# Kernel tuning notes

Hardware: AMD Instinct MI355X
Metric: run time of the kernel (lower is better)

## Reference

```python
import jax, jax.numpy as jnp
import numpy as np
from jax import lax

B, T, C = 64, 1024, 512
INIT_P = 1.0
CLAMP_LO, CLAMP_HI = 1e-4, 1.0 - 1e-4


def setup_inputs() -> dict:
    key = jax.random.key(0)
    k1, k2 = jax.random.split(key)
    x = jax.random.normal(k1, (B, T, C), dtype=jnp.float32)
    # learnable per-channel logit(lambda); original inits to logit(0.98) repeated,
    # use randn around that value so gradients are nontrivial
    init_logit = float(np.log(0.98 / (1.0 - 0.98)))
    logit_lambda = init_logit + 0.1 * jax.random.normal(k2, (C,), dtype=jnp.float32)
    return {"x": x, "logit_lambda": logit_lambda}


def reference(x, logit_lambda):
    # lam: [C] -> broadcast over (B, C) states
    lam = jnp.clip(jax.nn.sigmoid(logit_lambda), CLAMP_LO, CLAMP_HI)
    theta0 = x[:, 0, :]                                   # [B, C]
    P0 = jnp.full(theta0.shape, INIT_P, dtype=x.dtype)    # [B, C]

    def step(carry, xt):
        theta, P = carry
        K = P / (lam + P)                 # gain, data-independent of x
        theta = theta + K * (xt - theta)  # level update
        P = (P - K * P) / lam             # covariance update
        return (theta, P), theta

    xs = jnp.swapaxes(x, 0, 1)[1:]        # [T-1, B, C], timesteps 1..T-1
    _, ys = lax.scan(step, (theta0, P0), xs)
    # y[:,0,:] = x[:,0,:], y[:,t,:] = theta_t for t>=1
    y = jnp.concatenate([theta0[:, None, :], jnp.swapaxes(ys, 0, 1)], axis=1)
    return y
```

## Files before the change

kernel.cpp:

```cpp
#include <hip/hip_runtime.h>
#include <math.h>


namespace {
constexpr int kB = 64;
constexpr int kT = 1024;
constexpr int kC = 512;
constexpr int kNCH = 32;
constexpr int kL = kT / kNCH;
constexpr int kCV = kC / 4;
}

typedef float vfloat4 __attribute__((ext_vector_type(4)));

__device__ __forceinline__ void load_lam(const float* __restrict__ zl, int c0,
                                         float lam[4]) {
  vfloat4 z = *reinterpret_cast<const vfloat4*>(zl + c0);
#pragma unroll
  for (int k = 0; k < 4; ++k) {
    float s = 1.0f / (1.0f + expf(-z[k]));
    lam[k] = fminf(fmaxf(s, 1e-4f), 1.0f - 1e-4f);
  }
}

extern "C" __global__ __launch_bounds__(256) void ewrls_carry(
    const float* __restrict__ x, const float* __restrict__ zl,
    vfloat4* __restrict__ carry) {
  int idx = blockIdx.x * 256 + threadIdx.x;
  int cv = idx % kCV;
  int bj = idx / kCV;
  int j = bj % (kNCH - 1);
  int b = bj / (kNCH - 1);
  float lam[4];
  load_lam(zl, cv * 4, lam);

  const vfloat4* xp = reinterpret_cast<const vfloat4*>(x) +
                      ((size_t)b * kT + (size_t)j * kL) * kCV + cv;
  float s0 = 0.f, s1 = 0.f, s2 = 0.f, s3 = 0.f;
#pragma unroll 8
  for (int t = 0; t < kL; ++t) {
    vfloat4 v = xp[(size_t)t * kCV];
    s0 = fmaf(lam[0], s0, v.x);
    s1 = fmaf(lam[1], s1, v.y);
    s2 = fmaf(lam[2], s2, v.z);
    s3 = fmaf(lam[3], s3, v.w);
  }
  vfloat4 cr = {s0, s1, s2, s3};
  carry[((size_t)b * kNCH + j) * kCV + cv] = cr;
}

extern "C" __global__ __launch_bounds__(256) void ewrls_out(
    const float* __restrict__ x, const float* __restrict__ zl,
    const vfloat4* __restrict__ carry, float* __restrict__ y) {
  int idx = blockIdx.x * 256 + threadIdx.x;
  int cv = idx % kCV;
  int bj = idx / kCV;
  int j = bj % kNCH;
  int b = bj / kNCH;
  float lam[4];
  load_lam(zl, cv * 4, lam);

  float lamL[4];
#pragma unroll
  for (int k = 0; k < 4; ++k) {
    float p = lam[k];
#pragma unroll
    for (int q = 0; q < 5; ++q) p = p * p;
    lamL[k] = p;
  }

  float S[4] = {0.f, 0.f, 0.f, 0.f};
  float pj[4] = {1.f, 1.f, 1.f, 1.f};
  for (int i = 0; i < j; ++i) {
    vfloat4 cr = carry[((size_t)b * kNCH + i) * kCV + cv];
    S[0] = fmaf(lamL[0], S[0], cr.x);
    S[1] = fmaf(lamL[1], S[1], cr.y);
    S[2] = fmaf(lamL[2], S[2], cr.z);
    S[3] = fmaf(lamL[3], S[3], cr.w);
    pj[0] *= lamL[0];
    pj[1] *= lamL[1];
    pj[2] *= lamL[2];
    pj[3] *= lamL[3];
  }

  float Q[4];
#pragma unroll
  for (int k = 0; k < 4; ++k)
    Q[k] = (1.0f - pj[k]) * __builtin_amdgcn_rcpf(1.0f - lam[k]);

  const size_t base = ((size_t)b * kT + (size_t)j * kL) * kCV + cv;
  const vfloat4* xp = reinterpret_cast<const vfloat4*>(x) + base;
  vfloat4* yp = reinterpret_cast<vfloat4*>(y) + base;
#pragma unroll 8
  for (int t = 0; t < kL; ++t) {
    vfloat4 v = __builtin_nontemporal_load(&xp[(size_t)t * kCV]);
    S[0] = fmaf(lam[0], S[0], v.x);
    S[1] = fmaf(lam[1], S[1], v.y);
    S[2] = fmaf(lam[2], S[2], v.z);
    S[3] = fmaf(lam[3], S[3], v.w);
    Q[0] = fmaf(lam[0], Q[0], 1.0f);
    Q[1] = fmaf(lam[1], Q[1], 1.0f);
    Q[2] = fmaf(lam[2], Q[2], 1.0f);
    Q[3] = fmaf(lam[3], Q[3], 1.0f);
    vfloat4 o;
    o.x = S[0] * __builtin_amdgcn_rcpf(Q[0]);
    o.y = S[1] * __builtin_amdgcn_rcpf(Q[1]);
    o.z = S[2] * __builtin_amdgcn_rcpf(Q[2]);
    o.w = S[3] * __builtin_amdgcn_rcpf(Q[3]);
    __builtin_nontemporal_store(o, &yp[(size_t)t * kCV]);
  }
}

extern "C" __global__ __launch_bounds__(256) void ewrls_serial(
    const float* __restrict__ x, const float* __restrict__ zl,
    float* __restrict__ y) {
  int idx = blockIdx.x * 256 + threadIdx.x;
  int cv = idx % kCV;
  int b = idx / kCV;
  float lam[4];
  load_lam(zl, cv * 4, lam);
  float S[4] = {0.f, 0.f, 0.f, 0.f};
  float Q[4] = {0.f, 0.f, 0.f, 0.f};
  const size_t base = (size_t)b * kT * kCV + cv;
  const vfloat4* xp = reinterpret_cast<const vfloat4*>(x) + base;
  vfloat4* yp = reinterpret_cast<vfloat4*>(y) + base;
#pragma unroll 4
  for (int t = 0; t < kT; ++t) {
    vfloat4 v = xp[(size_t)t * kCV];
    S[0] = fmaf(lam[0], S[0], v.x);
    S[1] = fmaf(lam[1], S[1], v.y);
    S[2] = fmaf(lam[2], S[2], v.z);
    S[3] = fmaf(lam[3], S[3], v.w);
    Q[0] = fmaf(lam[0], Q[0], 1.0f);
    Q[1] = fmaf(lam[1], Q[1], 1.0f);
    Q[2] = fmaf(lam[2], Q[2], 1.0f);
    Q[3] = fmaf(lam[3], Q[3], 1.0f);
    vfloat4 o;
    o.x = S[0] * __builtin_amdgcn_rcpf(Q[0]);
    o.y = S[1] * __builtin_amdgcn_rcpf(Q[1]);
    o.z = S[2] * __builtin_amdgcn_rcpf(Q[2]);
    o.w = S[3] * __builtin_amdgcn_rcpf(Q[3]);
    yp[(size_t)t * kCV] = o;
  }
}

extern "C" void kernel_launch(void* const* d_in, const int* in_sizes, int n_in,
                              void* d_out, int out_size, void* d_ws,
                              size_t ws_size, hipStream_t stream) {
  const float* x = (const float*)d_in[0];
  const float* zl = (const float*)d_in[1];
  float* y = (float*)d_out;

  const size_t need = (size_t)kB * kNCH * kCV * sizeof(vfloat4);
  if (ws_size >= need) {
    vfloat4* carry = (vfloat4*)d_ws;
    const int n1 = kB * (kNCH - 1) * kCV;
    ewrls_carry<<<n1 / 256, 256, 0, stream>>>(x, zl, carry);
    const int n2 = kB * kNCH * kCV;
    ewrls_out<<<n2 / 256, 256, 0, stream>>>(x, zl, carry, y);
  } else {
    const int n = kB * kCV;
    ewrls_serial<<<n / 256, 256, 0, stream>>>(x, zl, y);
  }
}
```

Baseline: 261.7 us.

## Fuse carry and output passes into single-pass decoupled lookback scan

Replaces the two-kernel chunked scan (carry pass, then output pass that re-reads x) with one fused kernel. Blocks take chunk IDs in order from an atomic counter, keep their chunk of x in registers, publish a chunk carry with a release flag, and spin-wait on flags from earlier chunks before writing output. This is meant to remove the second full read of x and one kernel boundary. In exchange it adds a small init kernel, spin-wait latency through the chain of predecessor chunks, and high register pressure from holding 32 vfloat4 values per thread.

```diff
diff --git a/kernel.cpp b/kernel.cpp
--- a/kernel.cpp
+++ b/kernel.cpp
@@ -9,6 +9,9 @@
 constexpr int kNCH = 32;
 constexpr int kL = kT / kNCH;
 constexpr int kCV = kC / 4;
+constexpr int kChunks = kB * kNCH;
+constexpr size_t kFlagsOffB = 1024;
+constexpr size_t kCarryOffB = 65536;
 }
 
 typedef float vfloat4 __attribute__((ext_vector_type(4)));
@@ -23,42 +26,62 @@
   }
 }
 
-extern "C" __global__ __launch_bounds__(256) void ewrls_carry(
+extern "C" __global__ __launch_bounds__(256) void ewrls_init(
+    unsigned* __restrict__ ws) {
+  int i = blockIdx.x * 256 + threadIdx.x;
+  if (i == 0) ws[0] = 0u;
+  if (i < kChunks) ws[kFlagsOffB / 4 + i] = 0u;
+}
+
+extern "C" __global__ __launch_bounds__(256, 2) void ewrls_fused(
     const float* __restrict__ x, const float* __restrict__ zl,
-    vfloat4* __restrict__ carry) {
-  int idx = blockIdx.x * 256 + threadIdx.x;
-  int cv = idx % kCV;
-  int bj = idx / kCV;
-  int j = bj % (kNCH - 1);
-  int b = bj / (kNCH - 1);
+    unsigned* __restrict__ ws, float* __restrict__ y) {
+  __shared__ unsigned sh_vt;
+  if (threadIdx.x == 0)
+    sh_vt = __hip_atomic_fetch_add(ws, 1u, __ATOMIC_RELAXED,
+                                   __HIP_MEMORY_SCOPE_AGENT);
+  __syncthreads();
+  const unsigned c = 2u * sh_vt + (threadIdx.x >> 7);
+  const int j = (int)(c >> 6);
+  const int b = (int)(c & 63u);
+  const int cv = threadIdx.x & 127;
+
+  unsigned* __restrict__ flags = ws + kFlagsOffB / 4;
+  vfloat4* __restrict__ carry =
+      reinterpret_cast<vfloat4*>(reinterpret_cast<char*>(ws) + kCarryOffB);
+
   float lam[4];
   load_lam(zl, cv * 4, lam);
 
-  const vfloat4* xp = reinterpret_cast<const vfloat4*>(x) +
-                      ((size_t)b * kT + (size_t)j * kL) * kCV + cv;
-  float s0 = 0.f, s1 = 0.f, s2 = 0.f, s3 = 0.f;
-#pragma unroll 8
+  const size_t base = ((size_t)b * kT + (size_t)j * kL) * kCV + cv;
+  const vfloat4* xp = reinterpret_cast<const vfloat4*>(x) + base;
+  vfloat4 xs[kL];
+#pragma unroll
+  for (int t = 0; t < kL; ++t) xs[t] = xp[(size_t)t * kCV];
+
+  float a0 = 0.f, a1 = 0.f, a2 = 0.f, a3 = 0.f;
+#pragma unroll
   for (int t = 0; t < kL; ++t) {
-    vfloat4 v = xp[(size_t)t * kCV];
-    s0 = fmaf(lam[0], s0, v.x);
-    s1 = fmaf(lam[1], s1, v.y);
-    s2 = fmaf(lam[2], s2, v.z);
-    s3 = fmaf(lam[3], s3, v.w);
+    a0 = fmaf(lam[0], a0, xs[t].x);
+    a1 = fmaf(lam[1], a1, xs[t].y);
+    a2 = fmaf(lam[2], a2, xs[t].z);
+    a3 = fmaf(lam[3], a3, xs[t].w);
   }
-  vfloat4 cr = {s0, s1, s2, s3};
-  carry[((size_t)b * kNCH + j) * kCV + cv] = cr;
-}
 
-extern "C" __global__ __launch_bounds__(256) void ewrls_out(
-    const float* __restrict__ x, const float* __restrict__ zl,
-    const vfloat4* __restrict__ carry, float* __restrict__ y) {
-  int idx = blockIdx.x * 256 + threadIdx.x;
-  int cv = idx % kCV;
-  int bj = idx / kCV;
-  int j = bj % kNCH;
-  int b = bj / kNCH;
-  float lam[4];
-  load_lam(zl, cv * 4, lam);
+  {
+    union { vfloat4 v; unsigned long long u[2]; } pk;
+    pk.v.x = a0; pk.v.y = a1; pk.v.z = a2; pk.v.w = a3;
+    unsigned long long* p = reinterpret_cast<unsigned long long*>(
+        carry + ((size_t)c * kCV + cv));
+    __hip_atomic_store(p + 0, pk.u[0], __ATOMIC_RELAXED,
+                       __HIP_MEMORY_SCOPE_AGENT);
+    __hip_atomic_store(p + 1, pk.u[1], __ATOMIC_RELAXED,
+                       __HIP_MEMORY_SCOPE_AGENT);
+  }
+  __syncthreads();
+  if ((threadIdx.x & 127) == 0)
+    __hip_atomic_store(flags + c, 1u, __ATOMIC_RELEASE,
+                       __HIP_MEMORY_SCOPE_AGENT);
 
   float lamL[4];
 #pragma unroll
@@ -69,44 +92,51 @@
     lamL[k] = p;
   }
 
-  float S[4] = {0.f, 0.f, 0.f, 0.f};
-  float pj[4] = {1.f, 1.f, 1.f, 1.f};
+  float S0 = 0.f, S1 = 0.f, S2 = 0.f, S3 = 0.f;
+  float p0 = 1.f, p1 = 1.f, p2 = 1.f, p3 = 1.f;
   for (int i = 0; i < j; ++i) {
-    vfloat4 cr = carry[((size_t)b * kNCH + i) * kCV + cv];
-    S[0] = fmaf(lamL[0], S[0], cr.x);
-    S[1] = fmaf(lamL[1], S[1], cr.y);
-    S[2] = fmaf(lamL[2], S[2], cr.z);
-    S[3] = fmaf(lamL[3], S[3], cr.w);
-    pj[0] *= lamL[0];
-    pj[1] *= lamL[1];
-    pj[2] *= lamL[2];
-    pj[3] *= lamL[3];
+    const unsigned ci = (unsigned)(i * kB + b);
+    while (__hip_atomic_load(flags + ci, __ATOMIC_ACQUIRE,
+                             __HIP_MEMORY_SCOPE_AGENT) == 0u)
+      __builtin_amdgcn_s_sleep(2);
+    union { vfloat4 v; unsigned long long u[2]; } pk;
+    const unsigned long long* p = reinterpret_cast<const unsigned long long*>(
+        carry + ((size_t)ci * kCV + cv));
+    pk.u[0] = __hip_atomic_load(p + 0, __ATOMIC_RELAXED,
+                                __HIP_MEMORY_SCOPE_AGENT);
+    pk.u[1] = __hip_atomic_load(p + 1, __ATOMIC_RELAXED,
+                                __HIP_MEMORY_SCOPE_AGENT);
+    S0 = fmaf(lamL[0], S0, pk.v.x);
+    S1 = fmaf(lamL[1], S1, pk.v.y);
+    S2 = fmaf(lamL[2], S2, pk.v.z);
+    S3 = fmaf(lamL[3], S3, pk.v.w);
+    p0 *= lamL[0];
+    p1 *= lamL[1];
+    p2 *= lamL[2];
+    p3 *= lamL[3];
   }
 
-  float Q[4];
+  float Q0 = (1.0f - p0) * __builtin_amdgcn_rcpf(1.0f - lam[0]);
+  float Q1 = (1.0f - p1) * __builtin_amdgcn_rcpf(1.0f - lam[1]);
+  float Q2 = (1.0f - p2) * __builtin_amdgcn_rcpf(1.0f - lam[2]);
+  float Q3 = (1.0f - p3) * __builtin_amdgcn_rcpf(1.0f - lam[3]);
+
+  vfloat4* yp = reinterpret_cast<vfloat4*>(y) + base;
 #pragma unroll
-  for (int k = 0; k < 4; ++k)
-    Q[k] = (1.0f - pj[k]) * __builtin_amdgcn_rcpf(1.0f - lam[k]);
-
-  const size_t base = ((size_t)b * kT + (size_t)j * kL) * kCV + cv;
-  const vfloat4* xp = reinterpret_cast<const vfloat4*>(x) + base;
-  vfloat4* yp = reinterpret_cast<vfloat4*>(y) + base;
-#pragma unroll 8
   for (int t = 0; t < kL; ++t) {
-    vfloat4 v = __builtin_nontemporal_load(&xp[(size_t)t * kCV]);
-    S[0] = fmaf(lam[0], S[0], v.x);
-    S[1] = fmaf(lam[1], S[1], v.y);
-    S[2] = fmaf(lam[2], S[2], v.z);
-    S[3] = fmaf(lam[3], S[3], v.w);
-    Q[0] = fmaf(lam[0], Q[0], 1.0f);
-    Q[1] = fmaf(lam[1], Q[1], 1.0f);
-    Q[2] = fmaf(lam[2], Q[2], 1.0f);
-    Q[3] = fmaf(lam[3], Q[3], 1.0f);
+    S0 = fmaf(lam[0], S0, xs[t].x);
+    S1 = fmaf(lam[1], S1, xs[t].y);
+    S2 = fmaf(lam[2], S2, xs[t].z);
+    S3 = fmaf(lam[3], S3, xs[t].w);
+    Q0 = fmaf(lam[0], Q0, 1.0f);
+    Q1 = fmaf(lam[1], Q1, 1.0f);
+    Q2 = fmaf(lam[2], Q2, 1.0f);
+    Q3 = fmaf(lam[3], Q3, 1.0f);
     vfloat4 o;
-    o.x = S[0] * __builtin_amdgcn_rcpf(Q[0]);
-    o.y = S[1] * __builtin_amdgcn_rcpf(Q[1]);
-    o.z = S[2] * __builtin_amdgcn_rcpf(Q[2]);
-    o.w = S[3] * __builtin_amdgcn_rcpf(Q[3]);
+    o.x = S0 * __builtin_amdgcn_rcpf(Q0);
+    o.y = S1 * __builtin_amdgcn_rcpf(Q1);
+    o.z = S2 * __builtin_amdgcn_rcpf(Q2);
+    o.w = S3 * __builtin_amdgcn_rcpf(Q3);
     __builtin_nontemporal_store(o, &yp[(size_t)t * kCV]);
   }
 }
@@ -151,13 +181,12 @@
   const float* zl = (const float*)d_in[1];
   float* y = (float*)d_out;
 
-  const size_t need = (size_t)kB * kNCH * kCV * sizeof(vfloat4);
+  const size_t need =
+      kCarryOffB + (size_t)kChunks * kCV * sizeof(vfloat4);
   if (ws_size >= need) {
-    vfloat4* carry = (vfloat4*)d_ws;
-    const int n1 = kB * (kNCH - 1) * kCV;
-    ewrls_carry<<<n1 / 256, 256, 0, stream>>>(x, zl, carry);
-    const int n2 = kB * kNCH * kCV;
-    ewrls_out<<<n2 / 256, 256, 0, stream>>>(x, zl, carry, y);
+    unsigned* ws = (unsigned*)d_ws;
+    ewrls_init<<<(kChunks + 255) / 256, 256, 0, stream>>>(ws);
+    ewrls_fused<<<kChunks / 2, 256, 0, stream>>>(x, zl, ws, y);
   } else {
     const int n = kB * kCV;
     ewrls_serial<<<n / 256, 256, 0, stream>>>(x, zl, y);
```

Measured after the change: 799.1 us. 205% more time.
